# Optimization experiments

Measured on AMD Instinct MI355X. Metric: run time of the kernel, lower is better.

Reference implementation:

```python
import jax, jax.numpy as jnp
import numpy as np

B, N, D, K = 128, 65536, 512, 5
RATIO = 0.5


def setup_inputs() -> dict:
    key = jax.random.key(0)
    k1, k2, k3 = jax.random.split(key, 3)
    return {
        "s_f": jax.random.normal(k1, (B, D), jnp.float32),
        "t_f": jax.random.normal(k2, (B, D), jnp.float32),
        "gallery": jax.random.normal(k3, (N, D), jnp.float32),
    }


def _l2_normalize(x):
    # F.normalize(p=2, dim=1) with eps=1e-12 clamp on the norm
    n = jnp.linalg.norm(x, axis=1, keepdims=True)
    return x / jnp.maximum(n, 1e-12)


def reference(s_f, t_f, gallery):
    m = int(D * RATIO)  # number of lowest-|product| channels kept per row
    t_n = _l2_normalize(t_f)        # [B, D]
    s_n = _l2_normalize(s_f)        # [B, D]
    g_n = _l2_normalize(gallery)    # [N, D]

    # cosine retrieval in float64, as in the original (t_f.double().mm(...))
    sims = jnp.einsum('bd,nd->bn', t_n.astype(jnp.float64), g_n.astype(jnp.float64))  # [B, N]
    _, top_idx = jax.lax.top_k(sims, K)  # descending sort, take first K -> [B, K]

    # gather the K nearest gallery rows for every batch sample
    neighbors = g_n[top_idx]                       # [B, K, D]
    dmat = jnp.abs(neighbors * s_n[:, None, :])    # [B, K, D]

    # per-row ascending sort; keep the m smallest channel indices
    low_idx = jnp.argsort(dmat, axis=-1)[..., :m]  # [B, K, m]

    # membership bitmask per (batch, k) row: channel c in its bottom-m set?
    member = jnp.zeros((B, K, D), dtype=bool)
    member = member.at[
        jnp.arange(B)[:, None, None],
        jnp.arange(K)[None, :, None],
        low_idx,
    ].set(True)

    # the original's iterative cat+unique+counts intersection == AND-reduce
    # of all membership sets, starting from the full index set arange(D)
    zero_out = jnp.all(member, axis=(0, 1))  # [D] bool

    # compactor mask: ones, with intersected filter indices zeroed
    mask = jnp.where(zero_out, 0.0, 1.0).astype(jnp.float32)  # [D]
    return mask
```

## Files before the change

### kernel.cpp

```cpp
#include <hip/hip_runtime.h>

#define B 128
#define N 65536
#define D 512
#define K 5
#define M 256
#define GPB 256
#define NBLK1 (N / GPB)
#define CHR 16
#define NCHK (GPB / CHR)

typedef __attribute__((ext_vector_type(8))) short short8;
typedef __attribute__((ext_vector_type(4))) float f32x4;
typedef __attribute__((address_space(1))) const unsigned char as1cu8;
typedef __attribute__((address_space(3))) unsigned char as3u8;

__device__ __forceinline__ unsigned int pack_bf2(float lo, float hi) {
    return __builtin_amdgcn_perm(__float_as_uint(hi), __float_as_uint(lo), 0x07060302u);
}

__device__ __forceinline__ void top5_insert(float v, int gi, float tv[K], int ti[K]) {
    if (v > tv[K - 1] || (v == tv[K - 1] && gi < ti[K - 1])) {
        tv[K - 1] = v; ti[K - 1] = gi;
        #pragma unroll
        for (int k = K - 1; k > 0; --k) {
            bool sw = (tv[k] > tv[k - 1]) || (tv[k] == tv[k - 1] && ti[k] < ti[k - 1]);
            if (sw) {
                float fv = tv[k]; tv[k] = tv[k - 1]; tv[k - 1] = fv;
                int fi = ti[k]; ti[k] = ti[k - 1]; ti[k - 1] = fi;
            }
        }
    }
}

__device__ __forceinline__ void pk_insert(float sp, float lst[K]) {
    if (sp > lst[K - 1]) {
        lst[K - 1] = sp;
        #pragma unroll
        for (int k = K - 1; k > 0; --k)
            if (lst[k] > lst[k - 1]) {
                float t2 = lst[k]; lst[k] = lst[k - 1]; lst[k - 1] = t2;
            }
    }
}

__global__ __launch_bounds__(1024) void k1_sims(const float* __restrict__ t_f,
                                                const float* __restrict__ gal,
                                                float2* __restrict__ partial) {
    __shared__ __align__(16) char gbuf[2][CHR * 2048];
    __shared__ __align__(16) float cbuf_c[2][16][256];
    __shared__ __align__(16) float cbuf_n[2][16][16];

    const int tid = threadIdx.x;
    const int blk = blockIdx.x;
    const int lane = tid & 63;
    const int w = tid >> 6;
    const int l15 = lane & 15;
    const int l4 = lane >> 4;
    const int bt = w & 7;
    const int kh = w >> 3;

    const char* gal_b = reinterpret_cast<const char*>(gal);
    const size_t rowbase = ((size_t)blk * GPB) * (D * 4);
    const int lsw = (lane * 16) ^ ((w & 7) << 4);

    auto DMA = [&](int c, int bi) {
        const char* s0 = gal_b + rowbase + ((size_t)c * CHR + w) * (D * 4) + lsw;
        char* d = &gbuf[bi][w * 2048];
        __builtin_amdgcn_global_load_lds((as1cu8*)s0, (as3u8*)d, 16, 0, 0);
        __builtin_amdgcn_global_load_lds((as1cu8*)(s0 + 1024), (as3u8*)(d + 1024), 16, 0, 0);
    };

    DMA(0, 0);

    short8 tfr[8];
    {
        const float* tp = t_f + (size_t)(bt * 16 + l15) * D + (kh * 8) * 32 + l4 * 8;
        #pragma unroll
        for (int j = 0; j < 8; ++j) {
            float4 a = *reinterpret_cast<const float4*>(tp + j * 32);
            float4 b = *reinterpret_cast<const float4*>(tp + j * 32 + 4);
            uint4 q;
            q.x = pack_bf2(a.x, a.y); q.y = pack_bf2(a.z, a.w);
            q.z = pack_bf2(b.x, b.y); q.w = pack_bf2(b.z, b.w);
            tfr[j] = *reinterpret_cast<short8*>(&q);
        }
    }

    float lst[K];
    #pragma unroll
    for (int k = 0; k < K; ++k) lst[k] = -1e30f;

    const int xr = (l15 & 7) << 4;
    __syncthreads();

    for (int c = 0; c < NCHK; ++c) {
        const int bi = c & 1;
        if (c + 1 < NCHK) DMA(c + 1, bi ^ 1);

        if (c > 0 && kh == 1) {
            const int pb = bi ^ 1;
            f32x4 c0 = *reinterpret_cast<const f32x4*>(&cbuf_c[pb][bt][lane * 4]);
            f32x4 c1 = *reinterpret_cast<const f32x4*>(&cbuf_c[pb][8 + bt][lane * 4]);
            float4 n0 = *reinterpret_cast<const float4*>(&cbuf_n[pb][bt][l4 * 4]);
            float4 n1 = *reinterpret_cast<const float4*>(&cbuf_n[pb][8 + bt][l4 * 4]);
            float nn[4] = {n0.x + n1.x, n0.y + n1.y, n0.z + n1.z, n0.w + n1.w};
            #pragma unroll
            for (int r = 0; r < 4; ++r) {
                float s = (c0[r] + c1[r]) * rsqrtf(fmaxf(nn[r], 1e-24f));
                unsigned meta = (unsigned)((c - 1) * CHR + l4 * 4 + r);
                float sp = __uint_as_float((__float_as_uint(s) & 0xFFFFFF00u) | meta);
                pk_insert(sp, lst);
            }
        }

        f32x4 acc = (f32x4)0.0f;
        float nrm = 0.0f;
        const char* gb = &gbuf[bi][0];
        #pragma unroll
        for (int j = 0; j < 8; ++j) {
            const int ks = kh * 8 + j;
            const int base = l15 * 2048 + ks * 128;
            float4 a0 = *reinterpret_cast<const float4*>(gb + base + ((l4 * 32) ^ xr));
            float4 a1 = *reinterpret_cast<const float4*>(gb + base + ((l4 * 32 + 16) ^ xr));
            nrm = fmaf(a0.x, a0.x, nrm); nrm = fmaf(a0.y, a0.y, nrm);
            nrm = fmaf(a0.z, a0.z, nrm); nrm = fmaf(a0.w, a0.w, nrm);
            nrm = fmaf(a1.x, a1.x, nrm); nrm = fmaf(a1.y, a1.y, nrm);
            nrm = fmaf(a1.z, a1.z, nrm); nrm = fmaf(a1.w, a1.w, nrm);
            uint4 q;
            q.x = pack_bf2(a0.x, a0.y); q.y = pack_bf2(a0.z, a0.w);
            q.z = pack_bf2(a1.x, a1.y); q.w = pack_bf2(a1.z, a1.w);
            short8 af = *reinterpret_cast<short8*>(&q);
            acc = __builtin_amdgcn_mfma_f32_16x16x32_bf16(af, tfr[j], acc, 0, 0, 0);
        }
        nrm += __shfl_xor(nrm, 16);
        nrm += __shfl_xor(nrm, 32);
        if (lane < CHR) cbuf_n[bi][w][lane] = nrm;
        *reinterpret_cast<f32x4*>(&cbuf_c[bi][w][lane * 4]) = acc;

        __syncthreads();
    }

    if (kh == 1) {
        const int pb = (NCHK - 1) & 1;
        f32x4 c0 = *reinterpret_cast<const f32x4*>(&cbuf_c[pb][bt][lane * 4]);
        f32x4 c1 = *reinterpret_cast<const f32x4*>(&cbuf_c[pb][8 + bt][lane * 4]);
        float4 n0 = *reinterpret_cast<const float4*>(&cbuf_n[pb][bt][l4 * 4]);
        float4 n1 = *reinterpret_cast<const float4*>(&cbuf_n[pb][8 + bt][l4 * 4]);
        float nn[4] = {n0.x + n1.x, n0.y + n1.y, n0.z + n1.z, n0.w + n1.w};
        #pragma unroll
        for (int r = 0; r < 4; ++r) {
            float s = (c0[r] + c1[r]) * rsqrtf(fmaxf(nn[r], 1e-24f));
            unsigned meta = (unsigned)((NCHK - 1) * CHR + l4 * 4 + r);
            float sp = __uint_as_float((__float_as_uint(s) & 0xFFFFFF00u) | meta);
            pk_insert(sp, lst);
        }
    }

    #pragma unroll
    for (int mk = 16; mk <= 32; mk <<= 1) {
        float inc[K];
        #pragma unroll
        for (int k = 0; k < K; ++k) inc[k] = __shfl_xor(lst[k], mk);
        #pragma unroll
        for (int k = 0; k < K; ++k) pk_insert(inc[k], lst);
    }

    if (kh == 1 && l4 == 0) {
        const int b = bt * 16 + l15;
        #pragma unroll
        for (int k = 0; k < K; ++k) {
            unsigned sp = __float_as_uint(lst[k]);
            int g = blk * GPB + (int)(sp & 0xFFu);
            partial[((size_t)b * NBLK1 + blk) * K + k] = make_float2(lst[k], __int_as_float(g));
        }
    }
}

__global__ __launch_bounds__(512) void k2_merge(const float2* __restrict__ partial,
                                                int* __restrict__ top_idx) {
    __shared__ float2 wlist[8][K];
    const int b = blockIdx.x;
    const int p = threadIdx.x;
    const int lane = p & 63;
    const int w = p >> 6;

    float mv[K]; int mi[K];
    #pragma unroll
    for (int k = 0; k < K; ++k) { mv[k] = -1e30f; mi[k] = 0x7fffffff; }
    if (p < NBLK1) {
        #pragma unroll
        for (int k = 0; k < K; ++k) {
            float2 c = partial[((size_t)b * NBLK1 + p) * K + k];
            mv[k] = c.x; mi[k] = __float_as_int(c.y);
        }
    }
    #pragma unroll
    for (int mk = 1; mk <= 32; mk <<= 1) {
        float ov[K]; int oi[K];
        #pragma unroll
        for (int k = 0; k < K; ++k) { ov[k] = __shfl_xor(mv[k], mk); oi[k] = __shfl_xor(mi[k], mk); }
        #pragma unroll
        for (int k = 0; k < K; ++k) top5_insert(ov[k], oi[k], mv, mi);
    }
    if (lane == 0) {
        #pragma unroll
        for (int k = 0; k < K; ++k) wlist[w][k] = make_float2(mv[k], __int_as_float(mi[k]));
    }
    __syncthreads();
    if (w == 0) {
        #pragma unroll
        for (int k = 0; k < K; ++k) { mv[k] = -1e30f; mi[k] = 0x7fffffff; }
        if (lane < 8) {
            #pragma unroll
            for (int k = 0; k < K; ++k) {
                float2 c = wlist[lane][k];
                mv[k] = c.x; mi[k] = __float_as_int(c.y);
            }
        }
        #pragma unroll
        for (int mk = 1; mk <= 4; mk <<= 1) {
            float ov[K]; int oi[K];
            #pragma unroll
            for (int k = 0; k < K; ++k) { ov[k] = __shfl_xor(mv[k], mk); oi[k] = __shfl_xor(mi[k], mk); }
            #pragma unroll
            for (int k = 0; k < K; ++k) top5_insert(ov[k], oi[k], mv, mi);
        }
        if (lane == 0) {
            #pragma unroll
            for (int k = 0; k < K; ++k) top_idx[b * K + k] = mi[k];
        }
    }
}

__global__ __launch_bounds__(512) void k3_member(const float* __restrict__ s_f,
                                                 const float* __restrict__ gal,
                                                 const int* __restrict__ top_idx,
                                                 unsigned long long* __restrict__ bkmask) {
    __shared__ __align__(16) float pS[D];
    const int p = threadIdx.x;
    const int bk = blockIdx.x;
    const int b = bk / K;
    const int row = top_idx[bk];
    float pv = fabsf(gal[(size_t)row * D + p] * s_f[(size_t)b * D + p]);
    pS[p] = pv;
    __syncthreads();
    int cnt = 0;
    const float4* p4 = reinterpret_cast<const float4*>(pS);
    #pragma unroll 4
    for (int j = 0; j < D / 4; ++j) {
        float4 o = p4[j];
        cnt += (o.x < pv || (o.x == pv && (4 * j + 0) < p)) ? 1 : 0;
        cnt += (o.y < pv || (o.y == pv && (4 * j + 1) < p)) ? 1 : 0;
        cnt += (o.z < pv || (o.z == pv && (4 * j + 2) < p)) ? 1 : 0;
        cnt += (o.w < pv || (o.w == pv && (4 * j + 3) < p)) ? 1 : 0;
    }
    unsigned long long bm = __ballot(cnt < M);
    if ((p & 63) == 0) bkmask[(size_t)bk * 8 + (p >> 6)] = bm;
}

__global__ __launch_bounds__(512) void k4_final(const unsigned long long* __restrict__ bkmask,
                                                float* __restrict__ out) {
    __shared__ unsigned long long red[64][8];
    const int t = threadIdx.x;
    {
        const int word = t & 7, seg = t >> 3;
        unsigned long long acc = ~0ull;
        #pragma unroll
        for (int i = 0; i < 10; ++i)
            acc &= bkmask[(size_t)(seg * 10 + i) * 8 + word];
        red[seg][word] = acc;
    }
    __syncthreads();
    const int word = t >> 6, bit = t & 63;
    unsigned long long m = ~0ull;
    #pragma unroll 8
    for (int seg = 0; seg < 64; ++seg) m &= red[seg][word];
    out[t] = ((m >> bit) & 1ull) ? 0.0f : 1.0f;
}

extern "C" void kernel_launch(void* const* d_in, const int* in_sizes, int n_in,
                              void* d_out, int out_size, void* d_ws, size_t ws_size,
                              hipStream_t stream) {
    (void)in_sizes; (void)n_in; (void)out_size; (void)ws_size;
    const float* s_f = (const float*)d_in[0];
    const float* t_f = (const float*)d_in[1];
    const float* gal = (const float*)d_in[2];
    float* out = (float*)d_out;

    char* ws = (char*)d_ws;
    const size_t off_partial = 0;
    const size_t off_topidx  = off_partial + 1310720;
    const size_t off_bkmask  = off_topidx + 2560;

    float2* partial = (float2*)(ws + off_partial);
    int* top_idx = (int*)(ws + off_topidx);
    unsigned long long* bkmask = (unsigned long long*)(ws + off_bkmask);

    hipLaunchKernelGGL(k1_sims, dim3(NBLK1), dim3(1024), 0, stream, t_f, gal, partial);
    hipLaunchKernelGGL(k2_merge, dim3(B), dim3(512), 0, stream, partial, top_idx);
    hipLaunchKernelGGL(k3_member, dim3(B * K), dim3(512), 0, stream, s_f, gal, top_idx, bkmask);
    hipLaunchKernelGGL(k4_final, dim3(1), dim3(512), 0, stream, bkmask, out);
}
```

Before: 91.57 us.

## Combine split-K partials in-iteration via single-buffered LDS and own registers

Only the kh==0 waves write their MFMA partial and norm to shared memory. The kh==1 waves then read those after a barrier and add their own register accumulator and shuffled norm. This finalizes each chunk's scores in the same iteration rather than one iteration late. The goal is less LDS traffic and footprint and no epilogue. The cost is a second barrier per chunk and the kh==0 waves idling while kh==1 does the top-5 insertion.

New measurement: 99.66 us. 8.8% more time.

```diff
diff --git a/kernel.cpp b/kernel.cpp
--- a/kernel.cpp
+++ b/kernel.cpp
@@ -48,8 +48,8 @@
                                                 const float* __restrict__ gal,
                                                 float2* __restrict__ partial) {
     __shared__ __align__(16) char gbuf[2][CHR * 2048];
-    __shared__ __align__(16) float cbuf_c[2][16][256];
-    __shared__ __align__(16) float cbuf_n[2][16][16];
+    __shared__ __align__(16) float cbuf_c[8][256];
+    __shared__ __align__(16) float cbuf_n[16];
 
     const int tid = threadIdx.x;
     const int blk = blockIdx.x;
@@ -92,27 +92,11 @@
     for (int k = 0; k < K; ++k) lst[k] = -1e30f;
 
     const int xr = (l15 & 7) << 4;
-    __syncthreads();
 
     for (int c = 0; c < NCHK; ++c) {
         const int bi = c & 1;
+        __syncthreads();
         if (c + 1 < NCHK) DMA(c + 1, bi ^ 1);
-
-        if (c > 0 && kh == 1) {
-            const int pb = bi ^ 1;
-            f32x4 c0 = *reinterpret_cast<const f32x4*>(&cbuf_c[pb][bt][lane * 4]);
-            f32x4 c1 = *reinterpret_cast<const f32x4*>(&cbuf_c[pb][8 + bt][lane * 4]);
-            float4 n0 = *reinterpret_cast<const float4*>(&cbuf_n[pb][bt][l4 * 4]);
-            float4 n1 = *reinterpret_cast<const float4*>(&cbuf_n[pb][8 + bt][l4 * 4]);
-            float nn[4] = {n0.x + n1.x, n0.y + n1.y, n0.z + n1.z, n0.w + n1.w};
-            #pragma unroll
-            for (int r = 0; r < 4; ++r) {
-                float s = (c0[r] + c1[r]) * rsqrtf(fmaxf(nn[r], 1e-24f));
-                unsigned meta = (unsigned)((c - 1) * CHR + l4 * 4 + r);
-                float sp = __uint_as_float((__float_as_uint(s) & 0xFFFFFF00u) | meta);
-                pk_insert(sp, lst);
-            }
-        }
 
         f32x4 acc = (f32x4)0.0f;
         float nrm = 0.0f;
@@ -135,25 +119,28 @@
         }
         nrm += __shfl_xor(nrm, 16);
         nrm += __shfl_xor(nrm, 32);
-        if (lane < CHR) cbuf_n[bi][w][lane] = nrm;
-        *reinterpret_cast<f32x4*>(&cbuf_c[bi][w][lane * 4]) = acc;
-
-        __syncthreads();
-    }
-
-    if (kh == 1) {
-        const int pb = (NCHK - 1) & 1;
-        f32x4 c0 = *reinterpret_cast<const f32x4*>(&cbuf_c[pb][bt][lane * 4]);
-        f32x4 c1 = *reinterpret_cast<const f32x4*>(&cbuf_c[pb][8 + bt][lane * 4]);
-        float4 n0 = *reinterpret_cast<const float4*>(&cbuf_n[pb][bt][l4 * 4]);
-        float4 n1 = *reinterpret_cast<const float4*>(&cbuf_n[pb][8 + bt][l4 * 4]);
-        float nn[4] = {n0.x + n1.x, n0.y + n1.y, n0.z + n1.z, n0.w + n1.w};
-        #pragma unroll
-        for (int r = 0; r < 4; ++r) {
-            float s = (c0[r] + c1[r]) * rsqrtf(fmaxf(nn[r], 1e-24f));
-            unsigned meta = (unsigned)((NCHK - 1) * CHR + l4 * 4 + r);
-            float sp = __uint_as_float((__float_as_uint(s) & 0xFFFFFF00u) | meta);
-            pk_insert(sp, lst);
+
+        if (kh == 0) {
+            *reinterpret_cast<f32x4*>(&cbuf_c[bt][lane * 4]) = acc;
+            if (w == 0 && lane < CHR) cbuf_n[lane] = nrm;
+        }
+
+        asm volatile("s_waitcnt lgkmcnt(0)" ::: "memory");
+        __builtin_amdgcn_sched_barrier(0);
+        __builtin_amdgcn_s_barrier();
+        __builtin_amdgcn_sched_barrier(0);
+
+        if (kh == 1) {
+            f32x4 c0 = *reinterpret_cast<const f32x4*>(&cbuf_c[bt][lane * 4]);
+            float4 n0 = *reinterpret_cast<const float4*>(&cbuf_n[l4 * 4]);
+            #pragma unroll
+            for (int r = 0; r < 4; ++r) {
+                float nown = __shfl(nrm, l4 * 4 + r);
+                float s = (c0[r] + acc[r]) * rsqrtf(fmaxf(n0[r] + nown, 1e-24f));
+                unsigned meta = (unsigned)(c * CHR + l4 * 4 + r);
+                float sp = __uint_as_float((__float_as_uint(s) & 0xFFFFFF00u) | meta);
+                pk_insert(sp, lst);
+            }
         }
     }
 
```
